# Kernel tuning notes

Measured on AMD Instinct MI355X. Metric: run time of the kernel, lower is better.

Reference implementation:

```python
import jax, jax.numpy as jnp
import numpy as np

EMBED = 1024
HEAD = 128

def setup_inputs() -> dict:
    key = jax.random.key(0)
    k1, k2, k3, k4 = jax.random.split(key, 4)
    x = jax.random.normal(k1, (4, 4096, EMBED), dtype=jnp.float32)
    # nn.Linear default init ~ U(-1/sqrt(fan_in), 1/sqrt(fan_in)); weights stored as [in, out] for x @ W
    s = 1.0 / np.sqrt(EMBED)
    Wq = jax.random.uniform(k2, (EMBED, HEAD), dtype=jnp.float32, minval=-s, maxval=s)
    Wk = jax.random.uniform(k3, (EMBED, HEAD), dtype=jnp.float32, minval=-s, maxval=s)
    Wv = jax.random.uniform(k4, (EMBED, HEAD), dtype=jnp.float32, minval=-s, maxval=s)
    return {"x": x, "Wq": Wq, "Wk": Wk, "Wv": Wv}

def reference(x, Wq, Wk, Wv):
    # x: [B, S, E]
    B, S, E = x.shape
    q = x @ Wq  # [B, S, H]
    k = x @ Wk
    v = x @ Wv
    scale = jnp.asarray(k.shape[-1], x.dtype) ** -0.5
    scores = jnp.einsum('bqh,bkh->bqk', q, k) * scale  # [B, S, S]
    causal = jnp.tril(jnp.ones((S, S), dtype=bool))
    scores = jnp.where(causal, scores, jnp.asarray(-jnp.inf, x.dtype))
    attn = jax.nn.softmax(scores, axis=-1)
    return jnp.einsum('bqk,bkh->bqh', attn, v)  # [B, S, H]
```

## Files before the change

kernel.cpp:

```cpp
#include <hip/hip_runtime.h>
#include <math.h>

#define BATCH 4
#define SEQ   4096
#define EMB   1024
#define HD    128
#define MROWS (BATCH*SEQ)
#define SCALE  0.08838834764831844f
#define SCALEQ 0.12751742f
#define CHUNK 10
#define NJOBS 119
#define MAXC  7

typedef __attribute__((ext_vector_type(8))) short bf16x8;
typedef __attribute__((ext_vector_type(4))) short short4v;
typedef __attribute__((ext_vector_type(4))) float f32x4;
typedef __attribute__((ext_vector_type(4))) int   i32x4;
typedef __attribute__((ext_vector_type(2))) int   i32x2;

static __device__ __forceinline__ unsigned short f2bf(float f) {
    unsigned int u = __float_as_uint(f);
    u += 0x7fff + ((u >> 16) & 1);
    return (unsigned short)(u >> 16);
}
static __device__ __forceinline__ float bf2f(unsigned short s) {
    return __uint_as_float((unsigned int)s << 16);
}
static __device__ __forceinline__ short4v pack4(float4 a) {
    short4v p;
    p[0] = (short)f2bf(a.x); p[1] = (short)f2bf(a.y);
    p[2] = (short)f2bf(a.z); p[3] = (short)f2bf(a.w);
    return p;
}
static __device__ __forceinline__ int cvtpk(float lo, float hi) {
    int r;
    asm("v_cvt_pk_bf16_f32 %0, %1, %2" : "=v"(r) : "v"(lo), "v"(hi));
    return r;
}
static __device__ __forceinline__ void gload_lds16(const unsigned short* g, unsigned short* l) {
    __builtin_amdgcn_global_load_lds(
        (const __attribute__((address_space(1))) void*)g,
        (__attribute__((address_space(3))) void*)l, 16, 0, 0);
}

__global__ __launch_bounds__(256) void wtrans_kernel(
    const float* __restrict__ Wq, const float* __restrict__ Wk,
    const float* __restrict__ Wv, unsigned short* __restrict__ Wt)
{
    __shared__ __align__(16) unsigned short Xs[16 * 132];
    const int w  = blockIdx.y;
    const float* W = (w == 0) ? Wq : (w == 1) ? Wk : Wv;
    const float sc = (w == 0) ? SCALEQ : 1.0f;
    const int bx = blockIdx.x;
    const int k0 = bx * 16;
    const int t  = threadIdx.x;

#pragma unroll
    for (int i = 0; i < 2; ++i) {
        int gg = i * 256 + t;
        int row = gg >> 5, c4 = gg & 31;
        float4 a = *(const float4*)&W[(size_t)(k0 + row) * HD + c4 * 4];
        short4v p;
        p[0] = (short)f2bf(a.x * sc); p[1] = (short)f2bf(a.y * sc);
        p[2] = (short)f2bf(a.z * sc); p[3] = (short)f2bf(a.w * sc);
        *(short4v*)&Xs[row * 132 + c4 * 4] = p;
    }
    __syncthreads();
    const int n = t >> 1, g = t & 1;
    i32x4 o;
#pragma unroll
    for (int e = 0; e < 4; ++e) {
        unsigned int lo = Xs[(g * 8 + e * 2    ) * 132 + n];
        unsigned int hi = Xs[(g * 8 + e * 2 + 1) * 132 + n];
        o[e] = (int)(lo | (hi << 16));
    }
    const int ntg  = w * 8 + (n >> 4);
    const int kc   = bx >> 1;
    const int quad = (bx * 2 + g) & 3;
    const int lane = quad * 16 + (n & 15);
    *(i32x4*)&Wt[(((size_t)ntg * 32 + kc) * 64 + lane) * 8] = o;
}

__global__ __launch_bounds__(512, 2) void qkv_kernel(
    const float* __restrict__ x, const unsigned short* __restrict__ Wt,
    unsigned short* __restrict__ qb, unsigned short* __restrict__ kb,
    unsigned short* __restrict__ vtb)
{
    __shared__ __align__(1024) unsigned short lds[58368];
    unsigned short* Ws  = lds;
    unsigned short* xsA = lds + 49152;
    unsigned short* xsB = lds + 53760;

    const int t    = threadIdx.x;
    const int lane = t & 63, ng = t >> 6;
    const int quad = lane >> 4, l16 = lane & 15;
    const int m0   = blockIdx.x * 64;

    f32x4 acc[4][3];
#pragma unroll
    for (int i = 0; i < 4; ++i)
#pragma unroll
        for (int j = 0; j < 3; ++j) acc[i][j] = (f32x4){0.f, 0.f, 0.f, 0.f};

    const int xr0 = t >> 4,         xc0 = (t & 15) * 4;
    const int xr1 = (t + 512) >> 4, xc1 = ((t + 512) & 15) * 4;
    const float* xb0 = x + (size_t)(m0 + xr0) * EMB + xc0;
    const float* xb1 = x + (size_t)(m0 + xr1) * EMB + xc1;

    const unsigned short* Wg = Wt + (size_t)lane * 8;
    float4 xra, xrb;

    {
        float4 a = *(const float4*)&xb0[0];
        float4 b = *(const float4*)&xb1[0];
        *(short4v*)&xsA[xr0 * 72 + xc0] = pack4(a);
        *(short4v*)&xsA[xr1 * 72 + xc1] = pack4(b);
#pragma unroll
        for (int jt = 0; jt < 3; ++jt)
#pragma unroll
            for (int kcl = 0; kcl < 2; ++kcl) {
                int ntg = ng * 3 + jt;
                gload_lds16(Wg + ((size_t)ntg * 32 + kcl) * 512,
                            Ws + ((size_t)ntg * 2 + kcl) * 512);
            }
        xra = *(const float4*)&xb0[64];
        xrb = *(const float4*)&xb1[64];
    }
    asm volatile("s_waitcnt vmcnt(2)" ::: "memory");
    asm volatile("s_waitcnt lgkmcnt(0)" ::: "memory");
    __builtin_amdgcn_s_barrier();

    for (int ph = 0; ph < 16; ++ph) {
        const int cb = ph & 1, nb = cb ^ 1;
        unsigned short* xc = cb ? xsB : xsA;
        unsigned short* xn = cb ? xsA : xsB;
        const int kcn = (ph < 15 ? ph + 1 : 15) * 2;

#pragma unroll
        for (int jt = 0; jt < 3; ++jt)
#pragma unroll
            for (int kcl = 0; kcl < 2; ++kcl) {
                int ntg = ng * 3 + jt;
                gload_lds16(Wg + ((size_t)ntg * 32 + kcn + kcl) * 512,
                            Ws + ((size_t)(nb * 48) + ntg * 2 + kcl) * 512);
            }
        *(short4v*)&xn[xr0 * 72 + xc0] = pack4(xra);
        *(short4v*)&xn[xr1 * 72 + xc1] = pack4(xrb);
        {
            const int xcol = (ph + 2 < 16) ? (ph + 2) * 64 : 960;
            xra = *(const float4*)&xb0[xcol];
            xrb = *(const float4*)&xb1[xcol];
        }
        {
            bf16x8 aA[2][4], aB[2][3];
#pragma unroll
            for (int ks = 0; ks < 2; ++ks)
#pragma unroll
                for (int jt = 0; jt < 3; ++jt)
                    aB[ks][jt] = *(const bf16x8*)&Ws[((size_t)(cb * 48) + (ng * 3 + jt) * 2 + ks) * 512 + lane * 8];
#pragma unroll
            for (int ks = 0; ks < 2; ++ks)
#pragma unroll
                for (int mt = 0; mt < 4; ++mt)
                    aA[ks][mt] = *(const bf16x8*)&xc[(mt * 16 + l16) * 72 + ks * 32 + quad * 8];
            __builtin_amdgcn_s_setprio(1);
#pragma unroll
            for (int ks = 0; ks < 2; ++ks)
#pragma unroll
                for (int mt = 0; mt < 4; ++mt)
#pragma unroll
                    for (int jt = 0; jt < 3; ++jt)
                        acc[mt][jt] = __builtin_amdgcn_mfma_f32_16x16x32_bf16(
                            aA[ks][mt], aB[ks][jt], acc[mt][jt], 0, 0, 0);
            __builtin_amdgcn_s_setprio(0);
        }
        asm volatile("s_waitcnt vmcnt(2)" ::: "memory");
        asm volatile("s_waitcnt lgkmcnt(0)" ::: "memory");
        __builtin_amdgcn_s_barrier();
    }

    unsigned short* Cq = lds;
    unsigned short* Ck = lds + 64 * 136;
    unsigned short* Cv = lds + 2 * 64 * 136;
#pragma unroll
    for (int mt = 0; mt < 4; ++mt)
#pragma unroll
        for (int jt = 0; jt < 3; ++jt) {
            int nt = ng * 3 + jt;
            int wm = nt >> 3, nl = nt & 7;
            if (wm < 2) {
                unsigned short* C = (wm == 0) ? Cq : Ck;
#pragma unroll
                for (int rr = 0; rr < 4; ++rr)
                    C[(mt * 16 + quad * 4 + rr) * 136 + nl * 16 + l16] =
                        f2bf(acc[mt][jt][rr]);
            } else {
                i32x2 p;
                p[0] = cvtpk(acc[mt][jt][0], acc[mt][jt][1]);
                p[1] = cvtpk(acc[mt][jt][2], acc[mt][jt][3]);
                *(i32x2*)&Cv[(nl * 16 + l16) * 72 + mt * 16 + quad * 4] = p;
            }
        }
    __syncthreads();
    {
#pragma unroll
        for (int i = 0; i < 2; ++i) {
            int idx = i * 512 + t;
            int row = idx >> 4, seg = idx & 15;
            *(i32x4*)&qb[((size_t)(m0 + row)) * HD + seg * 8] = *(const i32x4*)&Cq[row * 136 + seg * 8];
            *(i32x4*)&kb[((size_t)(m0 + row)) * HD + seg * 8] = *(const i32x4*)&Ck[row * 136 + seg * 8];
        }
    }
    {
        const int b = m0 >> 12, s0 = m0 & 4095;
#pragma unroll
        for (int i = 0; i < 2; ++i) {
            int idx = i * 512 + t;
            int h = idx >> 3, seg = idx & 7;
            *(i32x4*)&vtb[(size_t)b * (HD * SEQ) + (size_t)h * SEQ + s0 + seg * 8] =
                *(const i32x4*)&Cv[h * 72 + seg * 8];
        }
    }
}

#define PADK 136
#define PADV 72
#define PADP 72
#define DEFER_THR 8.0f

__global__ __launch_bounds__(512, 4) void flash_kernel(
    const unsigned short* __restrict__ qb, const unsigned short* __restrict__ kb,
    const unsigned short* __restrict__ vtb, unsigned short* __restrict__ Opart,
    float* __restrict__ mbuf, float* __restrict__ lbuf)
{
    __shared__ __align__(16) unsigned short Ks[64 * PADK];
    __shared__ __align__(16) unsigned short Vt[128 * PADV];
    __shared__ __align__(16) unsigned short Pt[128 * PADP];

    const int bx   = blockIdx.x;
    const int slot = bx & 7, pp = bx >> 3;
    const int b    = slot >> 1;
    const int jj   = pp * 2 + (slot & 1);
    if (jj >= NJOBS) return;

    const int t    = threadIdx.x;
    const int lane = t & 63, w = t >> 6;
    const int quad = lane >> 4, l16 = lane & 15;

    int qi = 0, s = 0;
    for (qi = 0; qi < 32; ++qi) {
        int cnt = (qi + 5) / 5;
        if (jj < s + cnt) break;
        s += cnt;
    }
    const int c    = jj - s;
    const int qrow = qi * 128 + w * 16 + l16;
    const int jmax = 2 * qi + 2;
    const int jbeg = c * CHUNK;
    const int jend = min(jbeg + CHUNK, jmax);
    const int wtop = qi * 128 + w * 16;

    bf16x8 qf[4];
    {
        const unsigned short* qp = qb + ((size_t)b * SEQ + qrow) * HD;
#pragma unroll
        for (int ks = 0; ks < 4; ++ks)
            qf[ks] = *(const bf16x8*)&qp[ks * 32 + quad * 8];
    }

    f32x4 O[8];
#pragma unroll
    for (int i = 0; i < 8; ++i) O[i] = (f32x4){0.f, 0.f, 0.f, 0.f};
    float m_run = -1e30f, l_run = 0.f;

    const unsigned short* kbb  = kb  + (size_t)b * SEQ * HD;
    const unsigned short* vtbb = vtb + (size_t)b * HD * SEQ;

    const int gg0 = t, gg1 = 512 + t;
    i32x4 kr0, kr1, vr0, vr1;
    kr0 = *(const i32x4*)&kbb[(size_t)jbeg * 64 * HD + (size_t)gg0 * 8];
    kr1 = *(const i32x4*)&kbb[(size_t)jbeg * 64 * HD + (size_t)gg1 * 8];
    vr0 = *(const i32x4*)&vtbb[(size_t)(gg0 >> 3) * SEQ + jbeg * 64 + (gg0 & 7) * 8];
    vr1 = *(const i32x4*)&vtbb[(size_t)(gg1 >> 3) * SEQ + jbeg * 64 + (gg1 & 7) * 8];

    for (int j0 = jbeg; j0 < jend; ++j0) {
        __syncthreads();
        *(i32x4*)&Ks[(gg0 >> 4) * PADK + (gg0 & 15) * 8] = kr0;
        *(i32x4*)&Ks[(gg1 >> 4) * PADK + (gg1 & 15) * 8] = kr1;
        *(i32x4*)&Vt[(gg0 >> 3) * PADV + (gg0 & 7) * 8] = vr0;
        *(i32x4*)&Vt[(gg1 >> 3) * PADV + (gg1 & 7) * 8] = vr1;
        __syncthreads();

        if (j0 + 1 < jend) {
            const int j1 = j0 + 1;
            kr0 = *(const i32x4*)&kbb[(size_t)j1 * 64 * HD + (size_t)gg0 * 8];
            kr1 = *(const i32x4*)&kbb[(size_t)j1 * 64 * HD + (size_t)gg1 * 8];
            vr0 = *(const i32x4*)&vtbb[(size_t)(gg0 >> 3) * SEQ + j1 * 64 + (gg0 & 7) * 8];
            vr1 = *(const i32x4*)&vtbb[(size_t)(gg1 >> 3) * SEQ + j1 * 64 + (gg1 & 7) * 8];
        }

        if (j0 * 64 > wtop + 15) continue;

        f32x4 st[4];
        __builtin_amdgcn_s_setprio(1);
#pragma unroll
        for (int mt = 0; mt < 4; ++mt) {
            f32x4 a = (f32x4){0.f, 0.f, 0.f, 0.f};
#pragma unroll
            for (int ks = 0; ks < 4; ++ks) {
                bf16x8 kf = *(const bf16x8*)&Ks[(mt * 16 + l16) * PADK + ks * 32 + quad * 8];
                a = __builtin_amdgcn_mfma_f32_16x16x32_bf16(kf, qf[ks], a, 0, 0, 0);
            }
            st[mt] = a;
        }
        __builtin_amdgcn_s_setprio(0);

        if (j0 * 64 + 63 > wtop) {
#pragma unroll
            for (int mt = 0; mt < 4; ++mt)
#pragma unroll
                for (int rr = 0; rr < 4; ++rr) {
                    int kv = j0 * 64 + mt * 16 + quad * 4 + rr;
                    if (kv > qrow) st[mt][rr] = -1e30f;
                }
        }

        float mx = -1e30f;
#pragma unroll
        for (int mt = 0; mt < 4; ++mt)
#pragma unroll
            for (int rr = 0; rr < 4; ++rr) mx = fmaxf(mx, st[mt][rr]);
        mx = fmaxf(mx, __shfl_xor(mx, 16));
        mx = fmaxf(mx, __shfl_xor(mx, 32));
        if (!__all(mx <= m_run + DEFER_THR)) {
            const float m_new = fmaxf(m_run, mx);
            const float alpha = exp2f(m_run - m_new);
            l_run *= alpha;
#pragma unroll
            for (int i = 0; i < 8; ++i) {
                O[i][0] *= alpha; O[i][1] *= alpha; O[i][2] *= alpha; O[i][3] *= alpha;
            }
            m_run = m_new;
        }
        float psum = 0.f;
#pragma unroll
        for (int mt = 0; mt < 4; ++mt)
#pragma unroll
            for (int rr = 0; rr < 4; ++rr) {
                float p = exp2f(st[mt][rr] - m_run);
                st[mt][rr] = p;
                psum += p;
            }
        psum += __shfl_xor(psum, 16);
        psum += __shfl_xor(psum, 32);
        l_run += psum;

#pragma unroll
        for (int mt = 0; mt < 4; ++mt) {
            i32x2 p;
            p[0] = cvtpk(st[mt][0], st[mt][1]);
            p[1] = cvtpk(st[mt][2], st[mt][3]);
            *(i32x2*)&Pt[(w * 16 + l16) * PADP + mt * 16 + quad * 4] = p;
        }

        bf16x8 pf0 = *(const bf16x8*)&Pt[(w * 16 + l16) * PADP + quad * 8];
        bf16x8 pf1 = *(const bf16x8*)&Pt[(w * 16 + l16) * PADP + 32 + quad * 8];
        __builtin_amdgcn_s_setprio(1);
#pragma unroll
        for (int mt = 0; mt < 8; ++mt) {
            bf16x8 vf0 = *(const bf16x8*)&Vt[(mt * 16 + l16) * PADV + quad * 8];
            bf16x8 vf1 = *(const bf16x8*)&Vt[(mt * 16 + l16) * PADV + 32 + quad * 8];
            O[mt] = __builtin_amdgcn_mfma_f32_16x16x32_bf16(vf0, pf0, O[mt], 0, 0, 0);
            O[mt] = __builtin_amdgcn_mfma_f32_16x16x32_bf16(vf1, pf1, O[mt], 0, 0, 0);
        }
        __builtin_amdgcn_s_setprio(0);
    }

    const int r = w * 16 + l16;
    const size_t jobbase = (size_t)b * NJOBS + jj;
    unsigned short* po = Opart + jobbase * (128 * 128) + (size_t)r * 128;
#pragma unroll
    for (int mt = 0; mt < 8; ++mt) {
        i32x2 p;
        p[0] = cvtpk(O[mt][0], O[mt][1]);
        p[1] = cvtpk(O[mt][2], O[mt][3]);
        *(i32x2*)&po[mt * 16 + quad * 4] = p;
    }
    if (quad == 0) {
        mbuf[jobbase * 128 + r] = m_run;
        lbuf[jobbase * 128 + r] = l_run;
    }
}

__global__ __launch_bounds__(512) void combine_kernel(
    const unsigned short* __restrict__ Opart, const float* __restrict__ mbuf,
    const float* __restrict__ lbuf, float* __restrict__ out)
{
    const int qi = blockIdx.x, b = blockIdx.y;
    const int nc = (qi + 5) / 5;
    int j0 = 0;
    for (int q = 0; q < qi; ++q) j0 += (q + 5) / 5;
    const int t = threadIdx.x;
    const int row = blockIdx.z * 64 + (t >> 3);
    const int cg  = (t & 7) * 16;

    float mv[MAXC], lv[MAXC];
    float M = -1e30f;
#pragma unroll
    for (int c2 = 0; c2 < MAXC; ++c2) {
        if (c2 < nc) {
            const size_t jb = (size_t)b * NJOBS + j0 + c2;
            mv[c2] = mbuf[jb * 128 + row];
            lv[c2] = lbuf[jb * 128 + row];
            M = fmaxf(M, mv[c2]);
        } else { mv[c2] = -1e30f; lv[c2] = 0.f; }
    }
    float L = 0.f;
#pragma unroll
    for (int c2 = 0; c2 < MAXC; ++c2)
        if (c2 < nc) L += exp2f(mv[c2] - M) * lv[c2];
    const float Linv = 1.0f / L;

    float acc[16];
#pragma unroll
    for (int i = 0; i < 16; ++i) acc[i] = 0.f;
#pragma unroll
    for (int c2 = 0; c2 < MAXC; ++c2) {
        if (c2 < nc) {
            const float wgt = exp2f(mv[c2] - M) * Linv;
            const unsigned short* po = Opart + ((size_t)b * NJOBS + j0 + c2) * (128 * 128) +
                                       (size_t)row * 128 + cg;
#pragma unroll
            for (int i = 0; i < 2; ++i) {
                i32x4 d = *(const i32x4*)&po[i * 8];
#pragma unroll
                for (int e = 0; e < 4; ++e) {
                    unsigned int u = (unsigned int)d[e];
                    acc[i * 8 + e * 2]     = fmaf(wgt, bf2f((unsigned short)(u & 0xffff)), acc[i * 8 + e * 2]);
                    acc[i * 8 + e * 2 + 1] = fmaf(wgt, bf2f((unsigned short)(u >> 16)),   acc[i * 8 + e * 2 + 1]);
                }
            }
        }
    }
    float* op = out + ((size_t)b * SEQ + qi * 128 + row) * HD + cg;
#pragma unroll
    for (int i = 0; i < 4; ++i) {
        float4 res;
        res.x = acc[i * 4]; res.y = acc[i * 4 + 1];
        res.z = acc[i * 4 + 2]; res.w = acc[i * 4 + 3];
        *(float4*)&op[i * 4] = res;
    }
}

extern "C" void kernel_launch(void* const* d_in, const int* in_sizes, int n_in,
                              void* d_out, int out_size, void* d_ws, size_t ws_size,
                              hipStream_t stream) {
    const float* x  = (const float*)d_in[0];
    const float* Wq = (const float*)d_in[1];
    const float* Wk = (const float*)d_in[2];
    const float* Wv = (const float*)d_in[3];

    unsigned short* qb    = (unsigned short*)d_ws;
    unsigned short* kb    = qb  + (size_t)MROWS * HD;
    unsigned short* vtb   = kb  + (size_t)MROWS * HD;
    unsigned short* Wt    = vtb + (size_t)MROWS * HD;
    unsigned short* Opart = Wt  + (size_t)3 * HD * EMB;
    float* mbuf = (float*)(Opart + (size_t)BATCH * NJOBS * 128 * 128);
    float* lbuf = mbuf + (size_t)BATCH * NJOBS * 128;
    float* out = (float*)d_out;

    wtrans_kernel <<<dim3(64, 3),    dim3(256), 0, stream>>>(Wq, Wk, Wv, Wt);
    qkv_kernel    <<<dim3(256),      dim3(512), 0, stream>>>(x, Wt, qb, kb, vtb);
    flash_kernel  <<<dim3(480),      dim3(512), 0, stream>>>(qb, kb, vtb, Opart, mbuf, lbuf);
    combine_kernel<<<dim3(32, 4, 2), dim3(512), 0, stream>>>(Opart, mbuf, lbuf, out);
}
```

Before: 167.4 us.

## Load x fragments directly into registers and drop LDS double buffering in QKV GEMM

The QKV projection kernel stops staging x through LDS. Each lane now loads its own MFMA A-fragment rows from global memory and converts them to bf16 in registers. The W tiles are single-buffered, and the per-phase barrier is replaced by waitcnt plus sched_barrier. This shrinks LDS use and removes LDS traffic and barriers for x, which may allow higher occupancy. The cost is that the loads are no longer prefetched across phases, so global latency is exposed each iteration, and the 8 waves redundantly reload the same x rows. Without a barrier, the W buffer written by each wave's own lanes is reused only by that same wave, which is safe only because each wave loads its own ntg slices.

```diff
diff --git a/kernel.cpp b/kernel.cpp
--- a/kernel.cpp
+++ b/kernel.cpp
@@ -86,11 +86,7 @@
     unsigned short* __restrict__ qb, unsigned short* __restrict__ kb,
     unsigned short* __restrict__ vtb)
 {
-    __shared__ __align__(1024) unsigned short lds[58368];
-    unsigned short* Ws  = lds;
-    unsigned short* xsA = lds + 49152;
-    unsigned short* xsB = lds + 53760;
-
+    __shared__ __align__(1024) unsigned short lds[26624];
     const int t    = threadIdx.x;
     const int lane = t & 63, ng = t >> 6;
     const int quad = lane >> 4, l16 = lane & 15;
@@ -102,82 +98,71 @@
 #pragma unroll
         for (int j = 0; j < 3; ++j) acc[i][j] = (f32x4){0.f, 0.f, 0.f, 0.f};
 
-    const int xr0 = t >> 4,         xc0 = (t & 15) * 4;
-    const int xr1 = (t + 512) >> 4, xc1 = ((t + 512) & 15) * 4;
-    const float* xb0 = x + (size_t)(m0 + xr0) * EMB + xc0;
-    const float* xb1 = x + (size_t)(m0 + xr1) * EMB + xc1;
+    const float* xrow0 = x + (size_t)(m0 +  0 + l16) * EMB + quad * 8;
+    const float* xrow1 = x + (size_t)(m0 + 16 + l16) * EMB + quad * 8;
+    const float* xrow2 = x + (size_t)(m0 + 32 + l16) * EMB + quad * 8;
+    const float* xrow3 = x + (size_t)(m0 + 48 + l16) * EMB + quad * 8;
 
     const unsigned short* Wg = Wt + (size_t)lane * 8;
-    float4 xra, xrb;
-
-    {
-        float4 a = *(const float4*)&xb0[0];
-        float4 b = *(const float4*)&xb1[0];
-        *(short4v*)&xsA[xr0 * 72 + xc0] = pack4(a);
-        *(short4v*)&xsA[xr1 * 72 + xc1] = pack4(b);
+
+    for (int ph = 0; ph < 16; ++ph) {
+        const int kc = ph * 2;
 #pragma unroll
         for (int jt = 0; jt < 3; ++jt)
 #pragma unroll
             for (int kcl = 0; kcl < 2; ++kcl) {
                 int ntg = ng * 3 + jt;
-                gload_lds16(Wg + ((size_t)ntg * 32 + kcl) * 512,
-                            Ws + ((size_t)ntg * 2 + kcl) * 512);
-            }
-        xra = *(const float4*)&xb0[64];
-        xrb = *(const float4*)&xb1[64];
-    }
-    asm volatile("s_waitcnt vmcnt(2)" ::: "memory");
-    asm volatile("s_waitcnt lgkmcnt(0)" ::: "memory");
-    __builtin_amdgcn_s_barrier();
-
-    for (int ph = 0; ph < 16; ++ph) {
-        const int cb = ph & 1, nb = cb ^ 1;
-        unsigned short* xc = cb ? xsB : xsA;
-        unsigned short* xn = cb ? xsA : xsB;
-        const int kcn = (ph < 15 ? ph + 1 : 15) * 2;
-
-#pragma unroll
-        for (int jt = 0; jt < 3; ++jt)
-#pragma unroll
-            for (int kcl = 0; kcl < 2; ++kcl) {
-                int ntg = ng * 3 + jt;
-                gload_lds16(Wg + ((size_t)ntg * 32 + kcn + kcl) * 512,
-                            Ws + ((size_t)(nb * 48) + ntg * 2 + kcl) * 512);
-            }
-        *(short4v*)&xn[xr0 * 72 + xc0] = pack4(xra);
-        *(short4v*)&xn[xr1 * 72 + xc1] = pack4(xrb);
-        {
-            const int xcol = (ph + 2 < 16) ? (ph + 2) * 64 : 960;
-            xra = *(const float4*)&xb0[xcol];
-            xrb = *(const float4*)&xb1[xcol];
-        }
-        {
-            bf16x8 aA[2][4], aB[2][3];
-#pragma unroll
-            for (int ks = 0; ks < 2; ++ks)
+                gload_lds16(Wg + ((size_t)ntg * 32 + kc + kcl) * 512,
+                            lds + ((size_t)ntg * 2 + kcl) * 512);
+            }
+        const int col = ph * 64;
+        float4 xv[4][2][2];
+#pragma unroll
+        for (int ks = 0; ks < 2; ++ks) {
+            xv[0][ks][0] = *(const float4*)&xrow0[col + ks * 32];
+            xv[0][ks][1] = *(const float4*)&xrow0[col + ks * 32 + 4];
+            xv[1][ks][0] = *(const float4*)&xrow1[col + ks * 32];
+            xv[1][ks][1] = *(const float4*)&xrow1[col + ks * 32 + 4];
+            xv[2][ks][0] = *(const float4*)&xrow2[col + ks * 32];
+            xv[2][ks][1] = *(const float4*)&xrow2[col + ks * 32 + 4];
+            xv[3][ks][0] = *(const float4*)&xrow3[col + ks * 32];
+            xv[3][ks][1] = *(const float4*)&xrow3[col + ks * 32 + 4];
+        }
+        bf16x8 aA[2][4];
+#pragma unroll
+        for (int ks = 0; ks < 2; ++ks)
+#pragma unroll
+            for (int mt = 0; mt < 4; ++mt) {
+                i32x4 u;
+                u[0] = cvtpk(xv[mt][ks][0].x, xv[mt][ks][0].y);
+                u[1] = cvtpk(xv[mt][ks][0].z, xv[mt][ks][0].w);
+                u[2] = cvtpk(xv[mt][ks][1].x, xv[mt][ks][1].y);
+                u[3] = cvtpk(xv[mt][ks][1].z, xv[mt][ks][1].w);
+                aA[ks][mt] = *(bf16x8*)&u;
+            }
+        asm volatile("s_waitcnt vmcnt(0)" ::: "memory");
+        __builtin_amdgcn_sched_barrier(0);
+        bf16x8 aB[2][3];
+#pragma unroll
+        for (int ks = 0; ks < 2; ++ks)
+#pragma unroll
+            for (int jt = 0; jt < 3; ++jt)
+                aB[ks][jt] = *(const bf16x8*)&lds[((size_t)(ng * 3 + jt) * 2 + ks) * 512 + lane * 8];
+        asm volatile("s_waitcnt lgkmcnt(0)" ::: "memory");
+        __builtin_amdgcn_sched_barrier(0);
+        __builtin_amdgcn_s_setprio(1);
+#pragma unroll
+        for (int ks = 0; ks < 2; ++ks)
+#pragma unroll
+            for (int mt = 0; mt < 4; ++mt)
 #pragma unroll
                 for (int jt = 0; jt < 3; ++jt)
-                    aB[ks][jt] = *(const bf16x8*)&Ws[((size_t)(cb * 48) + (ng * 3 + jt) * 2 + ks) * 512 + lane * 8];
-#pragma unroll
-            for (int ks = 0; ks < 2; ++ks)
-#pragma unroll
-                for (int mt = 0; mt < 4; ++mt)
-                    aA[ks][mt] = *(const bf16x8*)&xc[(mt * 16 + l16) * 72 + ks * 32 + quad * 8];
-            __builtin_amdgcn_s_setprio(1);
-#pragma unroll
-            for (int ks = 0; ks < 2; ++ks)
-#pragma unroll
-                for (int mt = 0; mt < 4; ++mt)
-#pragma unroll
-                    for (int jt = 0; jt < 3; ++jt)
-                        acc[mt][jt] = __builtin_amdgcn_mfma_f32_16x16x32_bf16(
-                            aA[ks][mt], aB[ks][jt], acc[mt][jt], 0, 0, 0);
-            __builtin_amdgcn_s_setprio(0);
-        }
-        asm volatile("s_waitcnt vmcnt(2)" ::: "memory");
-        asm volatile("s_waitcnt lgkmcnt(0)" ::: "memory");
-        __builtin_amdgcn_s_barrier();
-    }
+                    acc[mt][jt] = __builtin_amdgcn_mfma_f32_16x16x32_bf16(
+                        aA[ks][mt], aB[ks][jt], acc[mt][jt], 0, 0, 0);
+        __builtin_amdgcn_s_setprio(0);
+    }
+
+    __syncthreads();
 
     unsigned short* Cq = lds;
     unsigned short* Ck = lds + 64 * 136;
```

After: 206.3 us. 1.23x slower.

## Give each flash wave two 16-row query tiles to reuse K/V fragments

Applied to the files above, without the earlier changes.

The flash kernel drops from 8 waves of 512 threads to 4 waves of 256 threads, and each wave now handles 32 query rows as two 16-row MFMA tiles. Every K and V fragment read from shared memory is used for two MFMAs, which halves LDS reads per unit of compute. Each thread now stages four K/V vectors per tile instead of two. The cost is much higher register pressure from doubled accumulators, Q fragments and score tiles, and the launch bound falls to 3 blocks per CU. Fewer waves per block may also hide latency less well, and causal skipping now happens at 32-row wave granularity, which wastes more work.

```diff
diff --git a/kernel.cpp b/kernel.cpp
--- a/kernel.cpp
+++ b/kernel.cpp
@@ -228,7 +228,7 @@
 #define PADP 72
 #define DEFER_THR 8.0f
 
-__global__ __launch_bounds__(512, 4) void flash_kernel(
+__global__ __launch_bounds__(256, 3) void flash_kernel(
     const unsigned short* __restrict__ qb, const unsigned short* __restrict__ kb,
     const unsigned short* __restrict__ vtb, unsigned short* __restrict__ Opart,
     float* __restrict__ mbuf, float* __restrict__ lbuf)
@@ -253,66 +253,81 @@
         if (jj < s + cnt) break;
         s += cnt;
     }
-    const int c    = jj - s;
-    const int qrow = qi * 128 + w * 16 + l16;
-    const int jmax = 2 * qi + 2;
-    const int jbeg = c * CHUNK;
-    const int jend = min(jbeg + CHUNK, jmax);
-    const int wtop = qi * 128 + w * 16;
-
-    bf16x8 qf[4];
+    const int c     = jj - s;
+    const int qrow0 = qi * 128 + w * 32 + l16;
+    const int qrow1 = qrow0 + 16;
+    const int jmax  = 2 * qi + 2;
+    const int jbeg  = c * CHUNK;
+    const int jend  = min(jbeg + CHUNK, jmax);
+    const int wtop  = qi * 128 + w * 32;
+
+    bf16x8 qf0[4], qf1[4];
     {
-        const unsigned short* qp = qb + ((size_t)b * SEQ + qrow) * HD;
-#pragma unroll
-        for (int ks = 0; ks < 4; ++ks)
-            qf[ks] = *(const bf16x8*)&qp[ks * 32 + quad * 8];
-    }
-
-    f32x4 O[8];
-#pragma unroll
-    for (int i = 0; i < 8; ++i) O[i] = (f32x4){0.f, 0.f, 0.f, 0.f};
-    float m_run = -1e30f, l_run = 0.f;
+        const unsigned short* qp0 = qb + ((size_t)b * SEQ + qrow0) * HD;
+        const unsigned short* qp1 = qb + ((size_t)b * SEQ + qrow1) * HD;
+#pragma unroll
+        for (int ks = 0; ks < 4; ++ks) {
+            qf0[ks] = *(const bf16x8*)&qp0[ks * 32 + quad * 8];
+            qf1[ks] = *(const bf16x8*)&qp1[ks * 32 + quad * 8];
+        }
+    }
+
+    f32x4 O0[8], O1[8];
+#pragma unroll
+    for (int i = 0; i < 8; ++i) {
+        O0[i] = (f32x4){0.f, 0.f, 0.f, 0.f};
+        O1[i] = (f32x4){0.f, 0.f, 0.f, 0.f};
+    }
+    float m0r = -1e30f, l0r = 0.f, m1r = -1e30f, l1r = 0.f;
 
     const unsigned short* kbb  = kb  + (size_t)b * SEQ * HD;
     const unsigned short* vtbb = vtb + (size_t)b * HD * SEQ;
 
-    const int gg0 = t, gg1 = 512 + t;
-    i32x4 kr0, kr1, vr0, vr1;
-    kr0 = *(const i32x4*)&kbb[(size_t)jbeg * 64 * HD + (size_t)gg0 * 8];
-    kr1 = *(const i32x4*)&kbb[(size_t)jbeg * 64 * HD + (size_t)gg1 * 8];
-    vr0 = *(const i32x4*)&vtbb[(size_t)(gg0 >> 3) * SEQ + jbeg * 64 + (gg0 & 7) * 8];
-    vr1 = *(const i32x4*)&vtbb[(size_t)(gg1 >> 3) * SEQ + jbeg * 64 + (gg1 & 7) * 8];
+    i32x4 kr[4], vr[4];
+#pragma unroll
+    for (int i = 0; i < 4; ++i) {
+        int gg = i * 256 + t;
+        kr[i] = *(const i32x4*)&kbb[(size_t)jbeg * 64 * HD + (size_t)gg * 8];
+        vr[i] = *(const i32x4*)&vtbb[(size_t)(gg >> 3) * SEQ + jbeg * 64 + (gg & 7) * 8];
+    }
 
     for (int j0 = jbeg; j0 < jend; ++j0) {
         __syncthreads();
-        *(i32x4*)&Ks[(gg0 >> 4) * PADK + (gg0 & 15) * 8] = kr0;
-        *(i32x4*)&Ks[(gg1 >> 4) * PADK + (gg1 & 15) * 8] = kr1;
-        *(i32x4*)&Vt[(gg0 >> 3) * PADV + (gg0 & 7) * 8] = vr0;
-        *(i32x4*)&Vt[(gg1 >> 3) * PADV + (gg1 & 7) * 8] = vr1;
+#pragma unroll
+        for (int i = 0; i < 4; ++i) {
+            int gg = i * 256 + t;
+            *(i32x4*)&Ks[(gg >> 4) * PADK + (gg & 15) * 8] = kr[i];
+            *(i32x4*)&Vt[(gg >> 3) * PADV + (gg & 7) * 8] = vr[i];
+        }
         __syncthreads();
 
         if (j0 + 1 < jend) {
             const int j1 = j0 + 1;
-            kr0 = *(const i32x4*)&kbb[(size_t)j1 * 64 * HD + (size_t)gg0 * 8];
-            kr1 = *(const i32x4*)&kbb[(size_t)j1 * 64 * HD + (size_t)gg1 * 8];
-            vr0 = *(const i32x4*)&vtbb[(size_t)(gg0 >> 3) * SEQ + j1 * 64 + (gg0 & 7) * 8];
-            vr1 = *(const i32x4*)&vtbb[(size_t)(gg1 >> 3) * SEQ + j1 * 64 + (gg1 & 7) * 8];
-        }
-
-        if (j0 * 64 > wtop + 15) continue;
-
-        f32x4 st[4];
+#pragma unroll
+            for (int i = 0; i < 4; ++i) {
+                int gg = i * 256 + t;
+                kr[i] = *(const i32x4*)&kbb[(size_t)j1 * 64 * HD + (size_t)gg * 8];
+                vr[i] = *(const i32x4*)&vtbb[(size_t)(gg >> 3) * SEQ + j1 * 64 + (gg & 7) * 8];
+            }
+        }
+
+        if (j0 * 64 > wtop + 31) continue;
+
+        f32x4 st0[4], st1[4];
+#pragma unroll
+        for (int mt = 0; mt < 4; ++mt) {
+            st0[mt] = (f32x4){0.f, 0.f, 0.f, 0.f};
+            st1[mt] = (f32x4){0.f, 0.f, 0.f, 0.f};
+        }
         __builtin_amdgcn_s_setprio(1);
 #pragma unroll
-        for (int mt = 0; mt < 4; ++mt) {
-            f32x4 a = (f32x4){0.f, 0.f, 0.f, 0.f};
+        for (int mt = 0; mt < 4; ++mt)
 #pragma unroll
             for (int ks = 0; ks < 4; ++ks) {
                 bf16x8 kf = *(const bf16x8*)&Ks[(mt * 16 + l16) * PADK + ks * 32 + quad * 8];
-                a = __builtin_amdgcn_mfma_f32_16x16x32_bf16(kf, qf[ks], a, 0, 0, 0);
-            }
-            st[mt] = a;
-        }
+                st0[mt] = __builtin_amdgcn_mfma_f32_16x16x32_bf16(kf, qf0[ks], st0[mt], 0, 0, 0);
+                st1[mt] = __builtin_amdgcn_mfma_f32_16x16x32_bf16(kf, qf1[ks], st1[mt], 0, 0, 0);
+            }
         __builtin_amdgcn_s_setprio(0);
 
         if (j0 * 64 + 63 > wtop) {
@@ -321,74 +336,132 @@
 #pragma unroll
                 for (int rr = 0; rr < 4; ++rr) {
                     int kv = j0 * 64 + mt * 16 + quad * 4 + rr;
-                    if (kv > qrow) st[mt][rr] = -1e30f;
+                    if (kv > qrow0) st0[mt][rr] = -1e30f;
+                    if (kv > qrow1) st1[mt][rr] = -1e30f;
                 }
         }
 
-        float mx = -1e30f;
-#pragma unroll
-        for (int mt = 0; mt < 4; ++mt)
-#pragma unroll
-            for (int rr = 0; rr < 4; ++rr) mx = fmaxf(mx, st[mt][rr]);
-        mx = fmaxf(mx, __shfl_xor(mx, 16));
-        mx = fmaxf(mx, __shfl_xor(mx, 32));
-        if (!__all(mx <= m_run + DEFER_THR)) {
-            const float m_new = fmaxf(m_run, mx);
-            const float alpha = exp2f(m_run - m_new);
-            l_run *= alpha;
-#pragma unroll
-            for (int i = 0; i < 8; ++i) {
-                O[i][0] *= alpha; O[i][1] *= alpha; O[i][2] *= alpha; O[i][3] *= alpha;
-            }
-            m_run = m_new;
-        }
-        float psum = 0.f;
-#pragma unroll
-        for (int mt = 0; mt < 4; ++mt)
-#pragma unroll
-            for (int rr = 0; rr < 4; ++rr) {
-                float p = exp2f(st[mt][rr] - m_run);
-                st[mt][rr] = p;
-                psum += p;
-            }
-        psum += __shfl_xor(psum, 16);
-        psum += __shfl_xor(psum, 32);
-        l_run += psum;
+        {
+            float mx = -1e30f;
+#pragma unroll
+            for (int mt = 0; mt < 4; ++mt)
+#pragma unroll
+                for (int rr = 0; rr < 4; ++rr) mx = fmaxf(mx, st0[mt][rr]);
+            mx = fmaxf(mx, __shfl_xor(mx, 16));
+            mx = fmaxf(mx, __shfl_xor(mx, 32));
+            if (!__all(mx <= m0r + DEFER_THR)) {
+                const float m_new = fmaxf(m0r, mx);
+                const float alpha = exp2f(m0r - m_new);
+                l0r *= alpha;
+#pragma unroll
+                for (int i = 0; i < 8; ++i) {
+                    O0[i][0] *= alpha; O0[i][1] *= alpha; O0[i][2] *= alpha; O0[i][3] *= alpha;
+                }
+                m0r = m_new;
+            }
+            float psum = 0.f;
+#pragma unroll
+            for (int mt = 0; mt < 4; ++mt)
+#pragma unroll
+                for (int rr = 0; rr < 4; ++rr) {
+                    float p = exp2f(st0[mt][rr] - m0r);
+                    st0[mt][rr] = p;
+                    psum += p;
+                }
+            psum += __shfl_xor(psum, 16);
+            psum += __shfl_xor(psum, 32);
+            l0r += psum;
+        }
+        {
+            float mx = -1e30f;
+#pragma unroll
+            for (int mt = 0; mt < 4; ++mt)
+#pragma unroll
+                for (int rr = 0; rr < 4; ++rr) mx = fmaxf(mx, st1[mt][rr]);
+            mx = fmaxf(mx, __shfl_xor(mx, 16));
+            mx = fmaxf(mx, __shfl_xor(mx, 32));
+            if (!__all(mx <= m1r + DEFER_THR)) {
+                const float m_new = fmaxf(m1r, mx);
+                const float alpha = exp2f(m1r - m_new);
+                l1r *= alpha;
+#pragma unroll
+                for (int i = 0; i < 8; ++i) {
+                    O1[i][0] *= alpha; O1[i][1] *= alpha; O1[i][2] *= alpha; O1[i][3] *= alpha;
+                }
+                m1r = m_new;
+            }
+            float psum = 0.f;
+#pragma unroll
+            for (int mt = 0; mt < 4; ++mt)
+#pragma unroll
+                for (int rr = 0; rr < 4; ++rr) {
+                    float p = exp2f(st1[mt][rr] - m1r);
+                    st1[mt][rr] = p;
+                    psum += p;
+                }
+            psum += __shfl_xor(psum, 16);
+            psum += __shfl_xor(psum, 32);
+            l1r += psum;
+        }
 
 #pragma unroll
         for (int mt = 0; mt < 4; ++mt) {
-            i32x2 p;
-            p[0] = cvtpk(st[mt][0], st[mt][1]);
-            p[1] = cvtpk(st[mt][2], st[mt][3]);
-            *(i32x2*)&Pt[(w * 16 + l16) * PADP + mt * 16 + quad * 4] = p;
-        }
-
-        bf16x8 pf0 = *(const bf16x8*)&Pt[(w * 16 + l16) * PADP + quad * 8];
-        bf16x8 pf1 = *(const bf16x8*)&Pt[(w * 16 + l16) * PADP + 32 + quad * 8];
+            i32x2 p0, p1;
+            p0[0] = cvtpk(st0[mt][0], st0[mt][1]);
+            p0[1] = cvtpk(st0[mt][2], st0[mt][3]);
+            p1[0] = cvtpk(st1[mt][0], st1[mt][1]);
+            p1[1] = cvtpk(st1[mt][2], st1[mt][3]);
+            *(i32x2*)&Pt[(w * 32 + l16) * PADP + mt * 16 + quad * 4] = p0;
+            *(i32x2*)&Pt[(w * 32 + 16 + l16) * PADP + mt * 16 + quad * 4] = p1;
+        }
+
+        bf16x8 pf00 = *(const bf16x8*)&Pt[(w * 32 + l16) * PADP + quad * 8];
+        bf16x8 pf01 = *(const bf16x8*)&Pt[(w * 32 + l16) * PADP + 32 + quad * 8];
+        bf16x8 pf10 = *(const bf16x8*)&Pt[(w * 32 + 16 + l16) * PADP + quad * 8];
+        bf16x8 pf11 = *(const bf16x8*)&Pt[(w * 32 + 16 + l16) * PADP + 32 + quad * 8];
         __builtin_amdgcn_s_setprio(1);
 #pragma unroll
         for (int mt = 0; mt < 8; ++mt) {
             bf16x8 vf0 = *(const bf16x8*)&Vt[(mt * 16 + l16) * PADV + quad * 8];
             bf16x8 vf1 = *(const bf16x8*)&Vt[(mt * 16 + l16) * PADV + 32 + quad * 8];
-            O[mt] = __builtin_amdgcn_mfma_f32_16x16x32_bf16(vf0, pf0, O[mt], 0, 0, 0);
-            O[mt] = __builtin_amdgcn_mfma_f32_16x16x32_bf16(vf1, pf1, O[mt], 0, 0, 0);
+            O0[mt] = __builtin_amdgcn_mfma_f32_16x16x32_bf16(vf0, pf00, O0[mt], 0, 0, 0);
+            O0[mt] = __builtin_amdgcn_mfma_f32_16x16x32_bf16(vf1, pf01, O0[mt], 0, 0, 0);
+            O1[mt] = __builtin_amdgcn_mfma_f32_16x16x32_bf16(vf0, pf10, O1[mt], 0, 0, 0);
+            O1[mt] = __builtin_amdgcn_mfma_f32_16x16x32_bf16(vf1, pf11, O1[mt], 0, 0, 0);
         }
         __builtin_amdgcn_s_setprio(0);
     }
 
-    const int r = w * 16 + l16;
     const size_t jobbase = (size_t)b * NJOBS + jj;
-    unsigned short* po = Opart + jobbase * (128 * 128) + (size_t)r * 128;
-#pragma unroll
-    for (int mt = 0; mt < 8; ++mt) {
-        i32x2 p;
-        p[0] = cvtpk(O[mt][0], O[mt][1]);
-        p[1] = cvtpk(O[mt][2], O[mt][3]);
-        *(i32x2*)&po[mt * 16 + quad * 4] = p;
-    }
-    if (quad == 0) {
-        mbuf[jobbase * 128 + r] = m_run;
-        lbuf[jobbase * 128 + r] = l_run;
+    {
+        const int r = w * 32 + l16;
+        unsigned short* po = Opart + jobbase * (128 * 128) + (size_t)r * 128;
+#pragma unroll
+        for (int mt = 0; mt < 8; ++mt) {
+            i32x2 p;
+            p[0] = cvtpk(O0[mt][0], O0[mt][1]);
+            p[1] = cvtpk(O0[mt][2], O0[mt][3]);
+            *(i32x2*)&po[mt * 16 + quad * 4] = p;
+        }
+        if (quad == 0) {
+            mbuf[jobbase * 128 + r] = m0r;
+            lbuf[jobbase * 128 + r] = l0r;
+        }
+    }
+    {
+        const int r = w * 32 + 16 + l16;
+        unsigned short* po = Opart + jobbase * (128 * 128) + (size_t)r * 128;
+#pragma unroll
+        for (int mt = 0; mt < 8; ++mt) {
+            i32x2 p;
+            p[0] = cvtpk(O1[mt][0], O1[mt][1]);
+            p[1] = cvtpk(O1[mt][2], O1[mt][3]);
+            *(i32x2*)&po[mt * 16 + quad * 4] = p;
+        }
+        if (quad == 0) {
+            mbuf[jobbase * 128 + r] = m1r;
+            lbuf[jobbase * 128 + r] = l1r;
+        }
     }
 }
 
@@ -471,6 +544,6 @@
 
     wtrans_kernel <<<dim3(64, 3),    dim3(256), 0, stream>>>(Wq, Wk, Wv, Wt);
     qkv_kernel    <<<dim3(256),      dim3(512), 0, stream>>>(x, Wt, qb, kb, vtb);
-    flash_kernel  <<<dim3(480),      dim3(512), 0, stream>>>(qb, kb, vtb, Opart, mbuf, lbuf);
+    flash_kernel  <<<dim3(480),      dim3(256), 0, stream>>>(qb, kb, vtb, Opart, mbuf, lbuf);
     combine_kernel<<<dim3(32, 4, 2), dim3(512), 0, stream>>>(Opart, mbuf, lbuf, out);
 }
```

Result: slower. 192.5 us (+15.0%).
